# Optimization experiments

Measured on AMD Instinct MI355X. Metric: run time of the kernel, lower is better.

Reference implementation:

```python
import jax, jax.numpy as jnp
import numpy as np

B, N, E, D, L, NC = 64, 128, 1024, 256, 2, 7
BETA = 0.3  # args.diffloss
BIG = 1e30  # mask_logic constant (score - (1-adj)*1e30), as in torch source lineage


def setup_inputs():
    key = jax.random.key(0)
    ks = iter(jax.random.split(key, 48))
    def p(shape, s=0.02):
        return jax.random.normal(next(ks), shape, jnp.float32) * s
    inp = {}
    inp["features"] = jax.random.normal(next(ks), (B, N, E), jnp.float32)
    inp["adj_1"] = jax.random.randint(next(ks), (B, N, N), 0, 2, jnp.int32)
    inp["adj_2"] = jax.random.randint(next(ks), (B, N, N), 0, 2, jnp.int32)
    inp["s_mask"] = jax.random.randint(next(ks), (B, N, N), 0, 2, jnp.int32)
    inp["s_mask_onehot"] = jnp.zeros((B, N, N, 2), jnp.int32)
    inp["lengths"] = jnp.full((B,), N, jnp.int32)
    inp["fc1_w"] = p((D, E)); inp["fc1_b"] = jnp.zeros((D,), jnp.float32)
    # GRUCell params (torch layout: weight_ih (3D,D) order r,z,n)
    for nm in ["gcs", "gps", "gcl", "gpl"]:
        inp[nm + "_wih"] = p((L, 3 * D, D)); inp[nm + "_whh"] = p((L, 3 * D, D))
        inp[nm + "_bih"] = jnp.zeros((L, 3 * D), jnp.float32)
        inp[nm + "_bhh"] = jnp.zeros((L, 3 * D), jnp.float32)
    # GatDot params per layer: linear1 (Q proj), linear2 (K proj)
    for nm in ["gats", "gatl"]:
        inp[nm + "_wq"] = p((L, D, D)); inp[nm + "_bq"] = jnp.zeros((L, D), jnp.float32)
        inp[nm + "_wk"] = p((L, D, D)); inp[nm + "_bk"] = jnp.zeros((L, D), jnp.float32)
    inp["affine1"] = p((2 * D, 2 * D), 0.05)
    inp["affine2"] = p((2 * D, 2 * D), 0.05)
    IN = 4 * D + E  # hidden*2*2 + emb_dim
    inp["mlp_w1"] = p((D, IN)); inp["mlp_b1"] = jnp.zeros((D,), jnp.float32)
    inp["mlp_w2"] = p((D, D)); inp["mlp_b2"] = jnp.zeros((D,), jnp.float32)
    inp["out_w"] = p((NC, D)); inp["out_b"] = jnp.zeros((NC,), jnp.float32)
    return inp


def gru_cell(x, h, wih, whh, bih, bhh):
    gi = x @ wih.T + bih
    gh = h @ whh.T + bhh
    ir, iz, in_ = jnp.split(gi, 3, axis=-1)
    hr, hz, hn = jnp.split(gh, 3, axis=-1)
    r = jax.nn.sigmoid(ir + hr)
    z = jax.nn.sigmoid(iz + hz)
    n = jnp.tanh(in_ + r * hn)
    return (1.0 - z) * n + z * h


def dag_pass(H_in, adj, gat, cpar, ppar):
    """Sequential DAG pass: per-utterance masked dot-product gather + GRU-C/GRU-P."""
    wq, bq, wk, bk = gat
    n = H_in.shape[1]
    idx = jnp.arange(n)

    def step(carry, inp):
        H1, Kb = carry            # H1: [B,N,D] written prefix; Kb = linear2(H1)
        i, x, arow = inp          # x: [B,D], arow: [B,N]
        q = x @ wq.T + bq
        scores = jnp.einsum('bnd,bd->bn', Kb, q)
        # torch: alpha - (1-adj)*1e30 over prefix :i; positions >= i excluded
        logits = scores - (1.0 - arow) * BIG - (idx >= i).astype(scores.dtype) * (2.0 * BIG)
        w = jax.nn.softmax(logits, axis=-1)
        M = jnp.einsum('bn,bnd->bd', w, H1)  # exactly 0 at i==0 (buffer zeros)
        C = gru_cell(x, M, *cpar)   # grus_c(input=x, hidden=M)
        P = gru_cell(M, x, *ppar)   # grus_p(input=M, hidden=x)
        h = C + P
        H1 = jax.lax.dynamic_update_slice(H1, h[:, None, :], (0, i, 0))
        Kb = jax.lax.dynamic_update_slice(Kb, (h @ wk.T + bk)[:, None, :], (0, i, 0))
        return (H1, Kb), None

    init = (jnp.zeros_like(H_in), jnp.zeros_like(H_in))
    xs = (idx, jnp.swapaxes(H_in, 0, 1), jnp.swapaxes(adj, 0, 1))
    (H1, _), _ = jax.lax.scan(step, init, xs)
    return H1


def diff_loss_fn(a, b):
    # orthogonality (DSN-style) loss between short/long channel features
    x = a.reshape(-1, a.shape[-1])
    y = b.reshape(-1, b.shape[-1])
    x = x - x.mean(axis=0, keepdims=True)
    y = y - y.mean(axis=0, keepdims=True)
    x = x / (jnp.linalg.norm(x, axis=1, keepdims=True) + 1e-6)
    y = y / (jnp.linalg.norm(y, axis=1, keepdims=True) + 1e-6)
    return jnp.mean((x.T @ y) ** 2)


def _forward(features, adj_1, adj_2,
             fc1_w, fc1_b,
             gcs_wih, gcs_whh, gcs_bih, gcs_bhh,
             gps_wih, gps_whh, gps_bih, gps_bhh,
             gcl_wih, gcl_whh, gcl_bih, gcl_bhh,
             gpl_wih, gpl_whh, gpl_bih, gpl_bhh,
             gats_wq, gats_bq, gats_wk, gats_bk,
             gatl_wq, gatl_bq, gatl_wk, gatl_bk,
             affine1, affine2,
             mlp_w1, mlp_b1, mlp_w2, mlp_b2, out_w, out_b):
    adj1 = adj_1.astype(jnp.float32)
    adj2 = adj_2.astype(jnp.float32)
    H0 = jax.nn.relu(features @ fc1_w.T + fc1_b)
    H0r = jax.nn.relu(features[:, ::-1] @ fc1_w.T + fc1_b)
    adj1r = adj1[:, ::-1, ::-1]
    adj2r = adj2[:, ::-1, ::-1]

    def channel(adjf, adjb, wq, bq, wk, bk, cwih, cwhh, cbih, cbhh, pwih, pwhh, pbih, pbhh):
        Hf, Hb = H0, H0r
        outs = []
        for l in range(L):
            gat = (wq[l], bq[l], wk[l], bk[l])
            cp = (cwih[l], cwhh[l], cbih[l], cbhh[l])
            pp = (pwih[l], pwhh[l], pbih[l], pbhh[l])
            Hf = dag_pass(Hf, adjf, gat, cp, pp)
            Hb = dag_pass(Hb, adjb, gat, cp, pp)
            outs.append(jnp.concatenate([Hf, Hb], axis=-1))  # no flip-back (as in source)
        return outs

    cs = channel(adj1, adj1r, gats_wq, gats_bq, gats_wk, gats_bk,
                 gcs_wih, gcs_whh, gcs_bih, gcs_bhh, gps_wih, gps_whh, gps_bih, gps_bhh)
    cl = channel(adj2, adj2r, gatl_wq, gatl_bq, gatl_wk, gatl_bk,
                 gcl_wih, gcl_whh, gcl_bih, gcl_bhh, gpl_wih, gpl_whh, gpl_bih, gpl_bhh)

    dloss = sum(diff_loss_fn(a, b) for a, b in zip(cs, cl)) * BETA

    HS, HL = cs[-1], cl[-1]  # [B,N,2D]
    A1 = jax.nn.softmax(jnp.einsum('bnd,de,bme->bnm', HS, affine1, HL), axis=-1)
    A2 = jax.nn.softmax(jnp.einsum('bnd,de,bme->bnm', HL, affine2, HS), axis=-1)
    HSn = jnp.einsum('bnm,bmd->bnd', A1, HL)
    HLn = jnp.einsum('bnm,bmd->bnd', A2, HS)

    Hfin = jnp.concatenate([features, HSn, HLn], axis=-1)  # in_dim = emb + 4D
    h = jax.nn.relu(Hfin @ mlp_w1.T + mlp_b1)
    h = jax.nn.relu(h @ mlp_w2.T + mlp_b2)
    logits = h @ out_w.T + out_b
    return logits, dloss


def reference(features, adj_1, adj_2, s_mask, s_mask_onehot, lengths,
              fc1_w, fc1_b,
              gcs_wih, gcs_whh, gcs_bih, gcs_bhh,
              gps_wih, gps_whh, gps_bih, gps_bhh,
              gcl_wih, gcl_whh, gcl_bih, gcl_bhh,
              gpl_wih, gpl_whh, gpl_bih, gpl_bhh,
              gats_wq, gats_bq, gats_wk, gats_bk,
              gatl_wq, gatl_bq, gatl_wk, gatl_bk,
              affine1, affine2,
              mlp_w1, mlp_b1, mlp_w2, mlp_b2, out_w, out_b):
    # s_mask / s_mask_onehot / lengths unused for attn_type='dotprod', no_rel_attn=True, nodal_att_type=None
    return _forward(features, adj_1, adj_2,
                    fc1_w, fc1_b,
                    gcs_wih, gcs_whh, gcs_bih, gcs_bhh,
                    gps_wih, gps_whh, gps_bih, gps_bhh,
                    gcl_wih, gcl_whh, gcl_bih, gcl_bhh,
                    gpl_wih, gpl_whh, gpl_bih, gpl_bhh,
                    gats_wq, gats_bq, gats_wk, gats_bk,
                    gatl_wq, gatl_bq, gatl_wk, gatl_bk,
                    affine1, affine2,
                    mlp_w1, mlp_b1, mlp_w2, mlp_b2, out_w, out_b)
```

## Files before the change

### kernel.cpp

```cpp
#include <hip/hip_runtime.h>
#include <hip/hip_fp16.h>
#include <math.h>

#define SB   64
#define SN   128
#define SE   1024
#define SD   256
#define SD2  512
#define SD3  768
#define SIN  2048
#define SNC  7
#define SBN  8192
#define CS   16

#define L_HS   0
#define L_GK   65536
#define L_XH   114688
#define L_QH   122880
#define L_ADJ  131072
#define L_MH   139264
#define L_LGP  139776
#define L_WGT  140800
#define L_S0   141312
#define SMEM_BYTES 141376

typedef _Float16 h2v __attribute__((ext_vector_type(2)));

__device__ __forceinline__ float wsum(float v){
#pragma unroll
  for (int o = 32; o; o >>= 1) v += __shfl_xor(v, o);
  return v;
}
__device__ __forceinline__ float sigm(float x){ return 1.f/(1.f + expf(-x)); }

__device__ __forceinline__ unsigned short f2h(float f){
  return __half_as_ushort(__float2half_rn(f));
}
__device__ __forceinline__ float h2f_(unsigned short u){
  return __half2float(__ushort_as_half(u));
}
__device__ __forceinline__ h2v u2h(unsigned u){
  union { unsigned u; h2v h; } c; c.u = u; return c.h;
}
__device__ __forceinline__ float dot8d(uint4 w, uint4 m, float acc){
  acc = __builtin_amdgcn_fdot2(u2h(w.x), u2h(m.x), acc, false);
  acc = __builtin_amdgcn_fdot2(u2h(w.y), u2h(m.y), acc, false);
  acc = __builtin_amdgcn_fdot2(u2h(w.z), u2h(m.z), acc, false);
  acc = __builtin_amdgcn_fdot2(u2h(w.w), u2h(m.w), acc, false);
  return acc;
}

template<bool BKMAJ, bool BIAS, bool RELU, bool ACC>
__global__ __launch_bounds__(256)
void gemm_k(const float* __restrict__ A, const float* __restrict__ Bm,
            const float* __restrict__ bias, float* __restrict__ C,
            int Nn, int K, int lda, int ldb, int ldc,
            long sA, long sB, long sC)
{
  __shared__ float As[16][132];
  __shared__ float Bs[16][68];
  const int t  = threadIdx.x;
  const int tx = t & 15, ty = t >> 4;
  const float* Ab = A + (long)blockIdx.z * sA;
  const float* Bb = Bm + (long)blockIdx.z * sB;
  float* Cb = C + (long)blockIdx.z * sC;
  const int m0 = blockIdx.y * 128, n0 = blockIdx.x * 64;
  float acc[8][4];
#pragma unroll
  for (int i = 0; i < 8; ++i)
#pragma unroll
    for (int j = 0; j < 4; ++j) acc[i][j] = 0.f;

  const int am = t >> 1, ak = (t & 1) * 8;
  int bn_ = 0, bk_ = 0;
  if (BKMAJ) { bk_ = t >> 4; bn_ = (t & 15) * 4; }
  else       { bn_ = t >> 2; bk_ = (t & 3) * 4; }

  for (int k0 = 0; k0 < K; k0 += 16) {
    const float4 a0 = *(const float4*)(Ab + (long)(m0 + am) * lda + k0 + ak);
    const float4 a1 = *(const float4*)(Ab + (long)(m0 + am) * lda + k0 + ak + 4);
    float4 b0;
    if (BKMAJ) b0 = *(const float4*)(Bb + (long)(k0 + bk_) * ldb + n0 + bn_);
    else       b0 = *(const float4*)(Bb + (long)(n0 + bn_) * ldb + k0 + bk_);
    __syncthreads();
    As[ak+0][am] = a0.x; As[ak+1][am] = a0.y; As[ak+2][am] = a0.z; As[ak+3][am] = a0.w;
    As[ak+4][am] = a1.x; As[ak+5][am] = a1.y; As[ak+6][am] = a1.z; As[ak+7][am] = a1.w;
    if (BKMAJ) { *(float4*)&Bs[bk_][bn_] = b0; }
    else { Bs[bk_+0][bn_] = b0.x; Bs[bk_+1][bn_] = b0.y; Bs[bk_+2][bn_] = b0.z; Bs[bk_+3][bn_] = b0.w; }
    __syncthreads();
#pragma unroll
    for (int kk = 0; kk < 16; ++kk) {
      float av[8], bv[4];
      *(float4*)&av[0] = *(const float4*)&As[kk][ty*8];
      *(float4*)&av[4] = *(const float4*)&As[kk][ty*8+4];
      *(float4*)&bv[0] = *(const float4*)&Bs[kk][tx*4];
#pragma unroll
      for (int ii = 0; ii < 8; ++ii)
#pragma unroll
        for (int jj = 0; jj < 4; ++jj)
          acc[ii][jj] = fmaf(av[ii], bv[jj], acc[ii][jj]);
    }
  }
#pragma unroll
  for (int ii = 0; ii < 8; ++ii) {
#pragma unroll
    for (int jj = 0; jj < 4; ++jj) {
      float v = acc[ii][jj];
      if (BIAS) v += bias[n0 + tx*4 + jj];
      const long ci = (long)(m0 + ty*8 + ii) * ldc + n0 + tx*4 + jj;
      if (ACC) v += Cb[ci];
      if (RELU) v = fmaxf(v, 0.f);
      Cb[ci] = v;
    }
  }
}

__global__ void spread_k(const float* __restrict__ src, float* __restrict__ xf,
                         float* __restrict__ xr)
{
  const int r = blockIdx.x, t = threadIdx.x;
  const int b = r >> 7, n = r & 127;
  const float v = src[(long)r * SD + t];
  xf[((long)(n * 64 + b)) * SD + t] = v;
  xr[((long)((127 - n) * 64 + b)) * SD + t] = v;
}

struct PTArgs { const float* wc[4]; const float* wp[4]; unsigned short* Wt; };
__global__ void packT_k(PTArgs a)
{
  const int kb8 = blockIdx.x, cd = blockIdx.y, t = threadIdx.x;
#pragma unroll
  for (int p = 0; p < 6; ++p) {
    const int r = t + 256 * p;
    const float* src = (r < 768) ? (a.wc[cd] + (long)r * SD)
                                 : (a.wp[cd] + (long)(r - 768) * SD);
    const float4 v0 = *(const float4*)(src + kb8 * 8);
    const float4 v1 = *(const float4*)(src + kb8 * 8 + 4);
    uint4 o;
    o.x = (unsigned)f2h(v0.x) | ((unsigned)f2h(v0.y) << 16);
    o.y = (unsigned)f2h(v0.z) | ((unsigned)f2h(v0.w) << 16);
    o.z = (unsigned)f2h(v1.x) | ((unsigned)f2h(v1.y) << 16);
    o.w = (unsigned)f2h(v1.z) | ((unsigned)f2h(v1.w) << 16);
    *(uint4*)(a.Wt + (((size_t)cd * 32 + kb8) * 1536 + r) * 8) = o;
  }
}

__global__ void s0_k(const float* __restrict__ Q, const float* __restrict__ bk,
                     float* __restrict__ S0)
{
  const int r = blockIdx.x * 4 + (threadIdx.x >> 6), lane = threadIdx.x & 63;
  const float4 q  = *(const float4*)(Q + (long)r * SD + lane * 4);
  const float4 kb = *(const float4*)(bk + lane * 4);
  float p = q.x*kb.x + q.y*kb.y + q.z*kb.z + q.w*kb.w;
  p = wsum(p);
  if (lane == 0) S0[r] = p;
}

struct StepArgs {
  const float* Qt[4]; const float* S0[4];
  const int* adj[4]; int rev[4];
  const float* bc[4];  const float* bp[4];
  const float* bgc[4]; const float* bgp[4];
  const float* X[4];
  float* H1[4];
  unsigned short* Hh;
  const unsigned short* Wt;
  const unsigned short* Wgk;
  int ldX, s0;
};
__global__ __launch_bounds__(256, 1) void step_chunk_k(StepArgs a)
{
  extern __shared__ __align__(16) char dsm[];
  unsigned short* Hs  = (unsigned short*)(dsm + L_HS);
  unsigned short* GKh = (unsigned short*)(dsm + L_GK);
  unsigned short* Xh  = (unsigned short*)(dsm + L_XH);
  unsigned short* Qh  = (unsigned short*)(dsm + L_QH);
  float* adjc = (float*)(dsm + L_ADJ);
  unsigned short* Mh  = (unsigned short*)(dsm + L_MH);
  float* lgp  = (float*)(dsm + L_LGP);
  float* wgt  = (float*)(dsm + L_WGT);
  float* s0s  = (float*)(dsm + L_S0);

  const int blk = blockIdx.x;
  const int cd = blk & 3, b = blk >> 2;
  const int t = threadIdx.x, j = t;
  const int ldX = a.ldX, c0 = a.s0;
  const float* Xp  = a.X[cd];
  float* H1 = a.H1[cd];
  unsigned short* Hg = a.Hh + ((size_t)(cd * 64 + b)) * 128 * 256;
  const float* Qtp = a.Qt[cd];
  const float* S0p = a.S0[cd];
  const int*   adjp = a.adj[cd];
  const int    rev  = a.rev[cd];

  const float bc0 = a.bc[cd][j],  bc1 = a.bc[cd][256+j],  bc2 = a.bc[cd][512+j];
  const float bp0 = a.bp[cd][j],  bp1 = a.bp[cd][256+j],  bp2 = a.bp[cd][512+j];

#pragma unroll
  for (int s = 0; s < CS; ++s) {
    Xh[s*256 + t] = f2h(Xp[((long)(c0+s)*64 + b)*ldX + t]);
    Qh[s*256 + t] = f2h(Qtp[((long)(c0+s)*64 + b)*SD + t]);
  }
  for (int z = t; z < CS*128; z += 256) {
    const int s = z >> 7, n = z & 127;
    const int i = c0 + s;
    int av = 0;
    if (i > 0) {
      const int ii = rev ? (SN-1-i) : i;
      const int nn = rev ? (SN-1-n) : n;
      av = adjp[((long)b*SN + ii)*SN + nn];
    }
    adjc[z] = (float)av;
  }
  if (t < CS) s0s[t] = S0p[(c0+t)*64 + b];
  for (int o = t*16; o < c0*512; o += 4096) {
    const uint4 v = *(const uint4*)((const char*)Hg + o);
    const int row = o >> 9, d2 = o & 511;
    *(uint4*)((char*)Hs + row*512 + (d2 ^ ((row & 31) << 4))) = v;
  }
  __syncthreads();

  {
    float gacc[6][CS];
#pragma unroll
    for (int g = 0; g < 6; ++g)
#pragma unroll
      for (int s = 0; s < CS; ++s) gacc[g][s] = 0.f;
    const unsigned short* wbase = a.Wgk + ((size_t)cd*32*1536 + j)*8;
    for (int kb8 = 0; kb8 < 32; ++kb8) {
      const uint4* wr = (const uint4*)(wbase + (size_t)kb8*12288);
      uint4 w[6];
#pragma unroll
      for (int g = 0; g < 6; ++g) w[g] = wr[g*256];
#pragma unroll
      for (int s = 0; s < CS; ++s) {
        const uint4 x8 = *(const uint4*)&Xh[s*256 + kb8*8];
#pragma unroll
        for (int g = 0; g < 6; ++g)
          gacc[g][s] = dot8d(w[g], x8, gacc[g][s]);
      }
    }
#pragma unroll
    for (int g = 0; g < 6; ++g) {
      const float bg = (g < 3) ? a.bgc[cd][g*256 + j] : a.bgp[cd][(g-3)*256 + j];
#pragma unroll
      for (int s = 0; s < CS; ++s)
        GKh[s*1536 + g*256 + j] = f2h(gacc[g][s] + bg);
    }
  }
  __syncthreads();

  for (int s = 0; s < CS; ++s) {
    const int i = c0 + s;
    float mreg = 0.f;
    if (i == 0) {
      Mh[t] = 0;
      __syncthreads();
    } else {
      {
        const int n = t & 127, hi = t >> 7;
        if (n < i) {
          const char* hrow = (const char*)Hs + n*512;
          const int cx = (n & 31) << 4;
          const unsigned short* qrow = Qh + s*256 + hi*128;
          float acc = 0.f;
#pragma unroll
          for (int k = 0; k < 16; ++k) {
            const uint4 hv = *(const uint4*)(hrow + (((hi*16 + k)*16) ^ cx));
            const uint4 qv = *(const uint4*)(qrow + k*8);
            acc = dot8d(hv, qv, acc);
          }
          lgp[t] = acc;
        }
      }
      __syncthreads();
      if (t < 64) {
        const float s0v = s0s[s];
        const int l = t;
        const float lg0 = lgp[l]      + lgp[128 + l];
        const float lg1 = lgp[64 + l] + lgp[192 + l];
        const float v0 = (l < i)    ? (lg0 + s0v - (1.f - adjc[s*128+l]   )*1e30f) : -3.0e38f;
        const float v1 = (l+64 < i) ? (lg1 + s0v - (1.f - adjc[s*128+l+64])*1e30f) : -3.0e38f;
        float mx = fmaxf(v0, v1);
#pragma unroll
        for (int o = 32; o; o >>= 1) mx = fmaxf(mx, __shfl_xor(mx, o));
        const float e0 = (l < i)    ? expf(v0 - mx) : 0.f;
        const float e1 = (l+64 < i) ? expf(v1 - mx) : 0.f;
        float sum = e0 + e1;
#pragma unroll
        for (int o = 32; o; o >>= 1) sum += __shfl_xor(sum, o);
        const float inv = 1.f / sum;
        if (l < i)    wgt[l]    = e0 * inv;
        if (l+64 < i) wgt[l+64] = e1 * inv;
      }
      __syncthreads();
      {
        float m0 = 0.f, m1 = 0.f, m2 = 0.f, m3 = 0.f;
        int n = 0;
        for (; n + 4 <= i; n += 4) {
          m0 = fmaf(wgt[n+0], h2f_(Hs[(n+0)*256 + (j ^ (((n+0)&31)<<3))]), m0);
          m1 = fmaf(wgt[n+1], h2f_(Hs[(n+1)*256 + (j ^ (((n+1)&31)<<3))]), m1);
          m2 = fmaf(wgt[n+2], h2f_(Hs[(n+2)*256 + (j ^ (((n+2)&31)<<3))]), m2);
          m3 = fmaf(wgt[n+3], h2f_(Hs[(n+3)*256 + (j ^ (((n+3)&31)<<3))]), m3);
        }
        for (; n < i; ++n)
          m0 = fmaf(wgt[n], h2f_(Hs[n*256 + (j ^ ((n&31)<<3))]), m0);
        mreg = (m0 + m1) + (m2 + m3);
        Mh[t] = f2h(mreg);
      }
      __syncthreads();
    }

    float g0 = 0.f, g1 = 0.f, g2 = 0.f, g3 = 0.f, g4 = 0.f, g5 = 0.f;
    {
      const unsigned short* wb = a.Wt + ((size_t)cd*32*1536 + j)*8;
      const uint4* wr0 = (const uint4*)wb;
      uint4 c0r = wr0[0], c1r = wr0[256], c2r = wr0[512],
            c3r = wr0[768], c4r = wr0[1024], c5r = wr0[1280];
#pragma unroll 4
      for (int kb8 = 0; kb8 < 32; ++kb8) {
        uint4 n0 = c0r, n1 = c1r, n2 = c2r, n3 = c3r, n4 = c4r, n5 = c5r;
        if (kb8 < 31) {
          const uint4* wn = (const uint4*)(wb + (size_t)(kb8+1)*12288);
          n0 = wn[0]; n1 = wn[256]; n2 = wn[512];
          n3 = wn[768]; n4 = wn[1024]; n5 = wn[1280];
        }
        const uint4 m8 = *(const uint4*)&Mh[kb8*8];
        g0 = dot8d(c0r, m8, g0);
        g1 = dot8d(c1r, m8, g1);
        g2 = dot8d(c2r, m8, g2);
        g3 = dot8d(c3r, m8, g3);
        g4 = dot8d(c4r, m8, g4);
        g5 = dot8d(c5r, m8, g5);
        c0r = n0; c1r = n1; c2r = n2; c3r = n3; c4r = n4; c5r = n5;
      }
    }
    {
      const int sb = s*1536;
      const float gic_r = h2f_(GKh[sb + j]);
      const float gic_z = h2f_(GKh[sb + 256 + j]);
      const float gic_n = h2f_(GKh[sb + 512 + j]);
      const float ghp_r = h2f_(GKh[sb + 768 + j]);
      const float ghp_z = h2f_(GKh[sb + 1024 + j]);
      const float ghp_n = h2f_(GKh[sb + 1280 + j]);
      const float xj = Xp[((long)i*64 + b)*ldX + j];
      const float rC = sigm(gic_r + g0 + bc0);
      const float zC = sigm(gic_z + g1 + bc1);
      const float nC = tanhf(gic_n + rC * (g2 + bc2));
      const float Cc = (1.f - zC) * nC + zC * mreg;
      const float rP = sigm(g3 + bp0 + ghp_r);
      const float zP = sigm(g4 + bp1 + ghp_z);
      const float nP = tanhf(g5 + bp2 + rP * ghp_n);
      const float hval = Cc + (1.f - zP) * nP + zP * xj;
      H1[((long)i*64 + b)*SD2 + j] = hval;
      const unsigned short hh = f2h(hval);
      Hs[i*256 + (j ^ ((i & 31) << 3))] = hh;
      Hg[(size_t)i*256 + j] = hh;
    }
    __syncthreads();
  }
}

__global__ void zero_k(float* p, long n)
{
  for (long idx = (long)blockIdx.x * 256 + threadIdx.x; idx < n; idx += (long)gridDim.x * 256)
    p[idx] = 0.f;
}

__global__ void colmean_k(const float* __restrict__ X, float* __restrict__ mean)
{
  __shared__ float red[256];
  const int c = blockIdx.x * 64 + (threadIdx.x & 63), rq = threadIdx.x >> 6;
  const int r0 = blockIdx.y * 256;
  float acc = 0.f;
  for (int r = r0 + rq; r < r0 + 256; r += 4) acc += X[(long)r * SD2 + c];
  red[threadIdx.x] = acc;
  __syncthreads();
  if (threadIdx.x < 64) {
    const float s = red[threadIdx.x] + red[64 + threadIdx.x] + red[128 + threadIdx.x] + red[192 + threadIdx.x];
    atomicAdd(&mean[c], s * (1.f / 8192.f));
  }
}

__global__ void rownorm_k(const float* __restrict__ X, const float* __restrict__ mean,
                          float* __restrict__ inv)
{
  const int r = blockIdx.x * 4 + (threadIdx.x >> 6), lane = threadIdx.x & 63;
  const float* xp = X + (long)r * SD2 + lane * 8;
  const float4 v0 = *(const float4*)xp;
  const float4 v1 = *(const float4*)(xp + 4);
  const float4 m0 = *(const float4*)(mean + lane * 8);
  const float4 m1 = *(const float4*)(mean + lane * 8 + 4);
  float ss = 0.f, d;
  d = v0.x - m0.x; ss += d*d;  d = v0.y - m0.y; ss += d*d;
  d = v0.z - m0.z; ss += d*d;  d = v0.w - m0.w; ss += d*d;
  d = v1.x - m1.x; ss += d*d;  d = v1.y - m1.y; ss += d*d;
  d = v1.z - m1.z; ss += d*d;  d = v1.w - m1.w; ss += d*d;
  ss = wsum(ss);
  if (lane == 0) inv[r] = 1.f / (sqrtf(ss) + 1e-6f);
}

__global__ __launch_bounds__(256)
void gpart_k(const float* __restrict__ X, const float* __restrict__ Y,
             const float* __restrict__ mx, const float* __restrict__ my,
             const float* __restrict__ ix, const float* __restrict__ iy,
             float* __restrict__ G)
{
  __shared__ float As[16][68];
  __shared__ float Bs[16][68];
  __shared__ float mxs[64], mys[64];
  const int t = threadIdx.x, tx = t & 15, ty = t >> 4;
  const int ci = blockIdx.y * 64, cj = blockIdx.x * 64;
  if (t < 64) { mxs[t] = mx[ci + t]; mys[t] = my[cj + t]; }
  float acc[4][4];
#pragma unroll
  for (int ii = 0; ii < 4; ++ii)
#pragma unroll
    for (int jj = 0; jj < 4; ++jj) acc[ii][jj] = 0.f;
  const int rl = t >> 4, c4 = (t & 15) * 4;
  __syncthreads();
  const int kend = blockIdx.z * 512 + 512;
  for (int kb = blockIdx.z * 512; kb < kend; kb += 16) {
    const int r = kb + rl;
    const float4 xv = *(const float4*)(X + (long)r * SD2 + ci + c4);
    const float4 yv = *(const float4*)(Y + (long)r * SD2 + cj + c4);
    const float vx = ix[r], vy = iy[r];
    __syncthreads();
    As[rl][c4+0] = (xv.x - mxs[c4+0]) * vx; As[rl][c4+1] = (xv.y - mxs[c4+1]) * vx;
    As[rl][c4+2] = (xv.z - mxs[c4+2]) * vx; As[rl][c4+3] = (xv.w - mxs[c4+3]) * vx;
    Bs[rl][c4+0] = (yv.x - mys[c4+0]) * vy; Bs[rl][c4+1] = (yv.y - mys[c4+1]) * vy;
    Bs[rl][c4+2] = (yv.z - mys[c4+2]) * vy; Bs[rl][c4+3] = (yv.w - mys[c4+3]) * vy;
    __syncthreads();
#pragma unroll
    for (int kk = 0; kk < 16; ++kk) {
      float av[4], bv[4];
      *(float4*)&av[0] = *(const float4*)&As[kk][ty*4];
      *(float4*)&bv[0] = *(const float4*)&Bs[kk][tx*4];
#pragma unroll
      for (int ii = 0; ii < 4; ++ii)
#pragma unroll
        for (int jj = 0; jj < 4; ++jj)
          acc[ii][jj] = fmaf(av[ii], bv[jj], acc[ii][jj]);
    }
  }
#pragma unroll
  for (int ii = 0; ii < 4; ++ii)
#pragma unroll
    for (int jj = 0; jj < 4; ++jj)
      atomicAdd(&G[(long)(ci + ty*4 + ii) * SD2 + cj + tx*4 + jj], acc[ii][jj]);
}

__global__ void sqsum_k(const float* __restrict__ G, float* __restrict__ dl)
{
  __shared__ float red[4];
  float s = 0.f;
  const long base = (long)blockIdx.x * 1024;
#pragma unroll
  for (int it = 0; it < 4; ++it) { const float v = G[base + it*256 + threadIdx.x]; s += v*v; }
  s = wsum(s);
  const int lane = threadIdx.x & 63, wv = threadIdx.x >> 6;
  if (lane == 0) red[wv] = s;
  __syncthreads();
  if (threadIdx.x == 0) atomicAdd(dl, red[0] + red[1] + red[2] + red[3]);
}

__global__ void smax_k(float* __restrict__ S)
{
  const int r = blockIdx.x * 4 + (threadIdx.x >> 6), lane = threadIdx.x & 63;
  float* p = S + (long)r * SN;
  const float v0 = p[lane], v1 = p[lane + 64];
  float mx = fmaxf(v0, v1);
#pragma unroll
  for (int o = 32; o; o >>= 1) mx = fmaxf(mx, __shfl_xor(mx, o));
  const float e0 = expf(v0 - mx), e1 = expf(v1 - mx);
  float s = e0 + e1;
#pragma unroll
  for (int o = 32; o; o >>= 1) s += __shfl_xor(s, o);
  const float inv = 1.f / s;
  p[lane] = e0 * inv; p[lane + 64] = e1 * inv;
}

__global__ void head_k(const float* __restrict__ H, const float* __restrict__ W,
                       const float* __restrict__ bo, float* __restrict__ out)
{
  const int r = blockIdx.x * 4 + (threadIdx.x >> 6), lane = threadIdx.x & 63;
  const float4 h = *(const float4*)(H + (long)r * SD + lane * 4);
#pragma unroll
  for (int c = 0; c < SNC; ++c) {
    const float4 w = *(const float4*)(W + (long)c * SD + lane * 4);
    float p = h.x*w.x + h.y*w.y + h.z*w.z + h.w*w.w;
    p = wsum(p);
    if (lane == 0) out[(long)r * SNC + c] = p + bo[c];
  }
}

__global__ void fin_k(const float* __restrict__ dl, float* __restrict__ out)
{
  out[0] = (dl[0] + dl[1]) * (0.3f / (512.f * 512.f));
}

extern "C" void kernel_launch(void* const* d_in, const int* in_sizes, int n_in,
                              void* d_out, int out_size, void* d_ws, size_t ws_size,
                              hipStream_t stream)
{
  (void)in_sizes; (void)n_in; (void)out_size; (void)ws_size;

  static bool attr_set = false;
  if (!attr_set) {
    hipFuncSetAttribute(reinterpret_cast<const void*>(step_chunk_k),
                        hipFuncAttributeMaxDynamicSharedMemorySize, SMEM_BYTES);
    attr_set = true;
  }

  const float* F    = (const float*)d_in[0];
  const int*   adj1 = (const int*)  d_in[1];
  const int*   adj2 = (const int*)  d_in[2];
  const float* fc1w = (const float*)d_in[6];
  const float* fc1b = (const float*)d_in[7];
  const float *g_wih[4], *g_whh[4], *g_bih[4], *g_bhh[4];
  for (int g = 0; g < 4; ++g) {
    g_wih[g] = (const float*)d_in[8 + g*4 + 0];
    g_whh[g] = (const float*)d_in[8 + g*4 + 1];
    g_bih[g] = (const float*)d_in[8 + g*4 + 2];
    g_bhh[g] = (const float*)d_in[8 + g*4 + 3];
  }
  const float* gat_wq[2] = {(const float*)d_in[24], (const float*)d_in[28]};
  const float* gat_bq[2] = {(const float*)d_in[25], (const float*)d_in[29]};
  const float* gat_wk[2] = {(const float*)d_in[26], (const float*)d_in[30]};
  const float* gat_bk[2] = {(const float*)d_in[27], (const float*)d_in[31]};
  const float* aff1 = (const float*)d_in[32];
  const float* aff2 = (const float*)d_in[33];
  const float* mw1  = (const float*)d_in[34];
  const float* mb1  = (const float*)d_in[35];
  const float* mw2  = (const float*)d_in[36];
  const float* mb2  = (const float*)d_in[37];
  const float* ow   = (const float*)d_in[38];
  const float* ob   = (const float*)d_in[39];
  float* out = (float*)d_out;

  float* ws = (float*)d_ws;
  size_t off = 0;
  auto take = [&](size_t nf){ float* p = ws + off; off += nf; return p; };
  float* region = take(22552576);
  float* X0f  = region;
  float* X0r  = region + 2097152;
  float* Qtb  = region + 4194304;
  float* Qtmp = region + 12582912;
  float* Htmp = region + 14680064;
  float* T  = region;
  float* Sb = region + 4194304;
  float* HH = region + 5242880;
  float* h1 = region + 9437184;
  float* h2 = region + 11534336;
  float* Ocat[2][2];
  for (int c = 0; c < 2; ++c) for (int l = 0; l < 2; ++l) Ocat[c][l] = take(4194304);
  float* S0b   = take(32768);
  unsigned short* WtB  = (unsigned short*)take(786432);
  unsigned short* WgkB = (unsigned short*)take(786432);
  unsigned short* HhB  = (unsigned short*)take(4194304);
  float* meanx = take(512);
  float* meany = take(512);
  float* invx  = take(8192);
  float* invy  = take(8192);
  float* dl    = take(8);
  float* Gbuf  = take(262144);

  gemm_k<false,true,true,false><<<dim3(4,64,1),256,0,stream>>>(
      F, fc1w, fc1b, Htmp, SD, SE, SE, SE, SD, 0,0,0);
  spread_k<<<SBN,256,0,stream>>>(Htmp, X0f, X0r);

  for (int l = 0; l < 2; ++l) {
    PTArgs pt, pg; StepArgs sta;
    sta.ldX = l ? SD2 : SD;
    sta.Wt = WtB; sta.Wgk = WgkB; sta.Hh = HhB;
    const int ldX = sta.ldX;
    for (int cd = 0; cd < 4; ++cd) {
      const int ch = cd >> 1;
      const float* X = (l == 0) ? ((cd & 1) ? X0r : X0f)
                                : (Ocat[ch][0] + (cd & 1) * SD);
      const float* wq   = gat_wq[ch] + l * SD * SD;
      const float* bq   = gat_bq[ch] + l * SD;
      const float* wk   = gat_wk[ch] + l * SD * SD;
      const float* bk   = gat_bk[ch] + l * SD;
      const float* cwih = g_wih[ch*2+0] + l * SD3 * SD;
      const float* cwhh = g_whh[ch*2+0] + l * SD3 * SD;
      const float* cbih = g_bih[ch*2+0] + l * SD3;
      const float* cbhh = g_bhh[ch*2+0] + l * SD3;
      const float* pwih = g_wih[ch*2+1] + l * SD3 * SD;
      const float* pwhh = g_whh[ch*2+1] + l * SD3 * SD;
      const float* pbih = g_bih[ch*2+1] + l * SD3;
      const float* pbhh = g_bhh[ch*2+1] + l * SD3;
      pt.wc[cd] = cwhh; pt.wp[cd] = pwih;
      pg.wc[cd] = cwih; pg.wp[cd] = pwhh;
      gemm_k<false,true,false,false><<<dim3(4,64,1),256,0,stream>>>(
          X, wq, bq, Qtmp, SD, SD, ldX, SD, SD, 0,0,0);
      gemm_k<true,false,false,false><<<dim3(4,64,1),256,0,stream>>>(
          Qtmp, wk, nullptr, Qtb + (size_t)cd*2097152, SD, SD, SD, SD, SD, 0,0,0);
      s0_k<<<SBN/4,256,0,stream>>>(Qtmp, bk, S0b + cd*SBN);
      float* H1mut = Ocat[ch][l] + (cd & 1) * SD;
      sta.Qt[cd] = Qtb + (size_t)cd*2097152;
      sta.S0[cd] = S0b + cd*SBN;
      sta.H1[cd] = H1mut;
      sta.adj[cd] = ch ? adj2 : adj1; sta.rev[cd] = cd & 1;
      sta.bc[cd]  = cbhh; sta.bp[cd]  = pbih;
      sta.bgc[cd] = cbih; sta.bgp[cd] = pbhh;
      sta.X[cd] = X;
    }
    pt.Wt = WtB;  packT_k<<<dim3(32,4),256,0,stream>>>(pt);
    pg.Wt = WgkB; packT_k<<<dim3(32,4),256,0,stream>>>(pg);

    for (int s0 = 0; s0 < SN; s0 += CS) {
      sta.s0 = s0;
      step_chunk_k<<<256,256,SMEM_BYTES,stream>>>(sta);
    }
  }

  zero_k<<<1,256,0,stream>>>(dl, 2);
  for (int l = 0; l < 2; ++l) {
    zero_k<<<4,256,0,stream>>>(meanx, 1024);
    colmean_k<<<dim3(8,32,1),256,0,stream>>>(Ocat[0][l], meanx);
    colmean_k<<<dim3(8,32,1),256,0,stream>>>(Ocat[1][l], meany);
    rownorm_k<<<SBN/4,256,0,stream>>>(Ocat[0][l], meanx, invx);
    rownorm_k<<<SBN/4,256,0,stream>>>(Ocat[1][l], meany, invy);
    zero_k<<<256,256,0,stream>>>(Gbuf, (long)SD2*SD2);
    gpart_k<<<dim3(8,8,16),256,0,stream>>>(Ocat[0][l], Ocat[1][l], meanx, meany, invx, invy, Gbuf);
    sqsum_k<<<256,256,0,stream>>>(Gbuf, dl + l);
  }

  gemm_k<true,false,false,false><<<dim3(8,64,1),256,0,stream>>>(
      Ocat[0][1], aff1, nullptr, T, SD2, SD2, SD2, SD2, SD2, 0,0,0);
  gemm_k<false,false,false,false><<<dim3(2,1,64),256,0,stream>>>(
      T, Ocat[1][1], nullptr, Sb, SN, SD2, 64*SD2, 64*SD2, SN, SD2, SD2, (long)SN*SN);
  smax_k<<<SBN/4,256,0,stream>>>(Sb);
  gemm_k<true,false,false,false><<<dim3(8,1,64),256,0,stream>>>(
      Sb, Ocat[1][1], nullptr, HH, SD2, SN, SN, 64*SD2, SD2, (long)SN*SN, SD2, (long)SN*SD2);
  gemm_k<false,true,false,false><<<dim3(4,64,1),256,0,stream>>>(
      F, mw1, mb1, h1, SD, SE, SE, SIN, SD, 0,0,0);
  gemm_k<false,false,false,true><<<dim3(4,64,1),256,0,stream>>>(
      HH, mw1 + 1024, nullptr, h1, SD, SD2, SD2, SIN, SD, 0,0,0);
  gemm_k<true,false,false,false><<<dim3(8,64,1),256,0,stream>>>(
      Ocat[1][1], aff2, nullptr, T, SD2, SD2, SD2, SD2, SD2, 0,0,0);
  gemm_k<false,false,false,false><<<dim3(2,1,64),256,0,stream>>>(
      T, Ocat[0][1], nullptr, Sb, SN, SD2, 64*SD2, 64*SD2, SN, SD2, SD2, (long)SN*SN);
  smax_k<<<SBN/4,256,0,stream>>>(Sb);
  gemm_k<true,false,false,false><<<dim3(8,1,64),256,0,stream>>>(
      Sb, Ocat[0][1], nullptr, HH, SD2, SN, SN, 64*SD2, SD2, (long)SN*SN, SD2, (long)SN*SD2);
  gemm_k<false,false,true,true><<<dim3(4,64,1),256,0,stream>>>(
      HH, mw1 + 1536, nullptr, h1, SD, SD2, SD2, SIN, SD, 0,0,0);
  gemm_k<false,true,true,false><<<dim3(4,64,1),256,0,stream>>>(
      h1, mw2, mb2, h2, SD, SD, SD, SD, SD, 0,0,0);
  head_k<<<SBN/4,256,0,stream>>>(h2, ow, ob, out);
  fin_k<<<1,1,0,stream>>>(dl, out + SBN * SNC);
}
```

Baseline: 4.743 ms.

## Double step kernel block size, splitting GRU-C and GRU-P gates across thread halves

```diff
diff --git a/kernel.cpp b/kernel.cpp
--- a/kernel.cpp
+++ b/kernel.cpp
@@ -20,9 +20,11 @@
 #define L_ADJ  131072
 #define L_MH   139264
 #define L_LGP  139776
-#define L_WGT  140800
-#define L_S0   141312
-#define SMEM_BYTES 141376
+#define L_MP   141824
+#define L_WGT  143872
+#define L_PBUF 144384
+#define L_S0   145408
+#define SMEM_BYTES 145472
 
 typedef _Float16 h2v __attribute__((ext_vector_type(2)));
 
@@ -168,7 +170,7 @@
   const unsigned short* Wgk;
   int ldX, s0;
 };
-__global__ __launch_bounds__(256, 1) void step_chunk_k(StepArgs a)
+__global__ __launch_bounds__(512, 1) void step_chunk_k(StepArgs a)
 {
   extern __shared__ __align__(16) char dsm[];
   unsigned short* Hs  = (unsigned short*)(dsm + L_HS);
@@ -178,12 +180,15 @@
   float* adjc = (float*)(dsm + L_ADJ);
   unsigned short* Mh  = (unsigned short*)(dsm + L_MH);
   float* lgp  = (float*)(dsm + L_LGP);
+  float* Mp   = (float*)(dsm + L_MP);
   float* wgt  = (float*)(dsm + L_WGT);
+  float* pbuf = (float*)(dsm + L_PBUF);
   float* s0s  = (float*)(dsm + L_S0);
 
   const int blk = blockIdx.x;
   const int cd = blk & 3, b = blk >> 2;
-  const int t = threadIdx.x, j = t;
+  const int t = threadIdx.x;
+  const int half = t >> 8, j = t & 255;
   const int ldX = a.ldX, c0 = a.s0;
   const float* Xp  = a.X[cd];
   float* H1 = a.H1[cd];
@@ -193,15 +198,23 @@
   const int*   adjp = a.adj[cd];
   const int    rev  = a.rev[cd];
 
-  const float bc0 = a.bc[cd][j],  bc1 = a.bc[cd][256+j],  bc2 = a.bc[cd][512+j];
-  const float bp0 = a.bp[cd][j],  bp1 = a.bp[cd][256+j],  bp2 = a.bp[cd][512+j];
-
-#pragma unroll
-  for (int s = 0; s < CS; ++s) {
-    Xh[s*256 + t] = f2h(Xp[((long)(c0+s)*64 + b)*ldX + t]);
-    Qh[s*256 + t] = f2h(Qtp[((long)(c0+s)*64 + b)*SD + t]);
-  }
-  for (int z = t; z < CS*128; z += 256) {
+  float eb0, eb1, eb2, gb0, gb1, gb2;
+  if (half == 0) {
+    eb0 = a.bc[cd][j];  eb1 = a.bc[cd][256+j];  eb2 = a.bc[cd][512+j];
+    gb0 = a.bgc[cd][j]; gb1 = a.bgc[cd][256+j]; gb2 = a.bgc[cd][512+j];
+  } else {
+    eb0 = a.bp[cd][j];  eb1 = a.bp[cd][256+j];  eb2 = a.bp[cd][512+j];
+    gb0 = a.bgp[cd][j]; gb1 = a.bgp[cd][256+j]; gb2 = a.bgp[cd][512+j];
+  }
+  const unsigned short* wb   = a.Wt  + ((size_t)cd*32*1536 + half*768 + j)*8;
+  const unsigned short* wbgk = a.Wgk + ((size_t)cd*32*1536 + half*768 + j)*8;
+
+  for (int z = t; z < CS*256; z += 512) {
+    const int s = z >> 8, c = z & 255;
+    Xh[z] = f2h(Xp[((long)(c0+s)*64 + b)*ldX + c]);
+    Qh[z] = f2h(Qtp[((long)(c0+s)*64 + b)*SD + c]);
+  }
+  for (int z = t; z < CS*128; z += 512) {
     const int s = z >> 7, n = z & 127;
     const int i = c0 + s;
     int av = 0;
@@ -213,7 +226,7 @@
     adjc[z] = (float)av;
   }
   if (t < CS) s0s[t] = S0p[(c0+t)*64 + b];
-  for (int o = t*16; o < c0*512; o += 4096) {
+  for (int o = t*16; o < c0*512; o += 8192) {
     const uint4 v = *(const uint4*)((const char*)Hg + o);
     const int row = o >> 9, d2 = o & 511;
     *(uint4*)((char*)Hs + row*512 + (d2 ^ ((row & 31) << 4))) = v;
@@ -221,52 +234,49 @@
   __syncthreads();
 
   {
-    float gacc[6][CS];
-#pragma unroll
-    for (int g = 0; g < 6; ++g)
+    float gacc[3][CS];
+#pragma unroll
+    for (int g = 0; g < 3; ++g)
 #pragma unroll
       for (int s = 0; s < CS; ++s) gacc[g][s] = 0.f;
-    const unsigned short* wbase = a.Wgk + ((size_t)cd*32*1536 + j)*8;
     for (int kb8 = 0; kb8 < 32; ++kb8) {
-      const uint4* wr = (const uint4*)(wbase + (size_t)kb8*12288);
-      uint4 w[6];
-#pragma unroll
-      for (int g = 0; g < 6; ++g) w[g] = wr[g*256];
+      const uint4* wr = (const uint4*)(wbgk + (size_t)kb8*12288);
+      const uint4 w0 = wr[0], w1 = wr[256], w2 = wr[512];
 #pragma unroll
       for (int s = 0; s < CS; ++s) {
         const uint4 x8 = *(const uint4*)&Xh[s*256 + kb8*8];
-#pragma unroll
-        for (int g = 0; g < 6; ++g)
-          gacc[g][s] = dot8d(w[g], x8, gacc[g][s]);
-      }
-    }
-#pragma unroll
-    for (int g = 0; g < 6; ++g) {
-      const float bg = (g < 3) ? a.bgc[cd][g*256 + j] : a.bgp[cd][(g-3)*256 + j];
+        gacc[0][s] = dot8d(w0, x8, gacc[0][s]);
+        gacc[1][s] = dot8d(w1, x8, gacc[1][s]);
+        gacc[2][s] = dot8d(w2, x8, gacc[2][s]);
+      }
+    }
+    const float gb[3] = {gb0, gb1, gb2};
+#pragma unroll
+    for (int g = 0; g < 3; ++g)
 #pragma unroll
       for (int s = 0; s < CS; ++s)
-        GKh[s*1536 + g*256 + j] = f2h(gacc[g][s] + bg);
-    }
+        GKh[s*1536 + (half*3 + g)*256 + j] = f2h(gacc[g][s] + gb[g]);
   }
   __syncthreads();
 
   for (int s = 0; s < CS; ++s) {
     const int i = c0 + s;
+    const float xj = Xp[((long)i*64 + b)*ldX + j];
     float mreg = 0.f;
     if (i == 0) {
-      Mh[t] = 0;
+      if (t < 256) Mh[t] = 0;
       __syncthreads();
     } else {
       {
-        const int n = t & 127, hi = t >> 7;
+        const int n = t & 127, q4 = t >> 7;
         if (n < i) {
           const char* hrow = (const char*)Hs + n*512;
           const int cx = (n & 31) << 4;
-          const unsigned short* qrow = Qh + s*256 + hi*128;
+          const unsigned short* qrow = Qh + s*256 + q4*64;
           float acc = 0.f;
 #pragma unroll
-          for (int k = 0; k < 16; ++k) {
-            const uint4 hv = *(const uint4*)(hrow + (((hi*16 + k)*16) ^ cx));
+          for (int k = 0; k < 8; ++k) {
+            const uint4 hv = *(const uint4*)(hrow + (((q4*8 + k)*16) ^ cx));
             const uint4 qv = *(const uint4*)(qrow + k*8);
             acc = dot8d(hv, qv, acc);
           }
@@ -277,8 +287,8 @@
       if (t < 64) {
         const float s0v = s0s[s];
         const int l = t;
-        const float lg0 = lgp[l]      + lgp[128 + l];
-        const float lg1 = lgp[64 + l] + lgp[192 + l];
+        const float lg0 = (lgp[l]      + lgp[128 + l]) + (lgp[256 + l] + lgp[384 + l]);
+        const float lg1 = (lgp[64 + l] + lgp[192 + l]) + (lgp[320 + l] + lgp[448 + l]);
         const float v0 = (l < i)    ? (lg0 + s0v - (1.f - adjc[s*128+l]   )*1e30f) : -3.0e38f;
         const float v1 = (l+64 < i) ? (lg1 + s0v - (1.f - adjc[s*128+l+64])*1e30f) : -3.0e38f;
         float mx = fmaxf(v0, v1);
@@ -296,68 +306,71 @@
       __syncthreads();
       {
         float m0 = 0.f, m1 = 0.f, m2 = 0.f, m3 = 0.f;
-        int n = 0;
-        for (; n + 4 <= i; n += 4) {
-          m0 = fmaf(wgt[n+0], h2f_(Hs[(n+0)*256 + (j ^ (((n+0)&31)<<3))]), m0);
-          m1 = fmaf(wgt[n+1], h2f_(Hs[(n+1)*256 + (j ^ (((n+1)&31)<<3))]), m1);
-          m2 = fmaf(wgt[n+2], h2f_(Hs[(n+2)*256 + (j ^ (((n+2)&31)<<3))]), m2);
-          m3 = fmaf(wgt[n+3], h2f_(Hs[(n+3)*256 + (j ^ (((n+3)&31)<<3))]), m3);
+        int n = half;
+        for (; n + 6 < i; n += 8) {
+          m0 = fmaf(wgt[n],   h2f_(Hs[(n  )*256 + (j ^ (((n  )&31)<<3))]), m0);
+          m1 = fmaf(wgt[n+2], h2f_(Hs[(n+2)*256 + (j ^ (((n+2)&31)<<3))]), m1);
+          m2 = fmaf(wgt[n+4], h2f_(Hs[(n+4)*256 + (j ^ (((n+4)&31)<<3))]), m2);
+          m3 = fmaf(wgt[n+6], h2f_(Hs[(n+6)*256 + (j ^ (((n+6)&31)<<3))]), m3);
         }
-        for (; n < i; ++n)
+        for (; n < i; n += 2)
           m0 = fmaf(wgt[n], h2f_(Hs[n*256 + (j ^ ((n&31)<<3))]), m0);
-        mreg = (m0 + m1) + (m2 + m3);
-        Mh[t] = f2h(mreg);
+        Mp[t] = (m0 + m1) + (m2 + m3);
       }
       __syncthreads();
-    }
-
-    float g0 = 0.f, g1 = 0.f, g2 = 0.f, g3 = 0.f, g4 = 0.f, g5 = 0.f;
+      if (half == 0) {
+        mreg = Mp[j] + Mp[256 + j];
+        Mh[j] = f2h(mreg);
+      }
+      __syncthreads();
+    }
+
+    float g0 = 0.f, g1 = 0.f, g2 = 0.f;
     {
-      const unsigned short* wb = a.Wt + ((size_t)cd*32*1536 + j)*8;
       const uint4* wr0 = (const uint4*)wb;
-      uint4 c0r = wr0[0], c1r = wr0[256], c2r = wr0[512],
-            c3r = wr0[768], c4r = wr0[1024], c5r = wr0[1280];
+      uint4 c0r = wr0[0], c1r = wr0[256], c2r = wr0[512];
 #pragma unroll 4
       for (int kb8 = 0; kb8 < 32; ++kb8) {
-        uint4 n0 = c0r, n1 = c1r, n2 = c2r, n3 = c3r, n4 = c4r, n5 = c5r;
+        uint4 n0 = c0r, n1 = c1r, n2 = c2r;
         if (kb8 < 31) {
           const uint4* wn = (const uint4*)(wb + (size_t)(kb8+1)*12288);
           n0 = wn[0]; n1 = wn[256]; n2 = wn[512];
-          n3 = wn[768]; n4 = wn[1024]; n5 = wn[1280];
         }
         const uint4 m8 = *(const uint4*)&Mh[kb8*8];
         g0 = dot8d(c0r, m8, g0);
         g1 = dot8d(c1r, m8, g1);
         g2 = dot8d(c2r, m8, g2);
-        g3 = dot8d(c3r, m8, g3);
-        g4 = dot8d(c4r, m8, g4);
-        g5 = dot8d(c5r, m8, g5);
-        c0r = n0; c1r = n1; c2r = n2; c3r = n3; c4r = n4; c5r = n5;
-      }
-    }
+        c0r = n0; c1r = n1; c2r = n2;
+      }
+    }
+
     {
       const int sb = s*1536;
-      const float gic_r = h2f_(GKh[sb + j]);
-      const float gic_z = h2f_(GKh[sb + 256 + j]);
-      const float gic_n = h2f_(GKh[sb + 512 + j]);
-      const float ghp_r = h2f_(GKh[sb + 768 + j]);
-      const float ghp_z = h2f_(GKh[sb + 1024 + j]);
-      const float ghp_n = h2f_(GKh[sb + 1280 + j]);
-      const float xj = Xp[((long)i*64 + b)*ldX + j];
-      const float rC = sigm(gic_r + g0 + bc0);
-      const float zC = sigm(gic_z + g1 + bc1);
-      const float nC = tanhf(gic_n + rC * (g2 + bc2));
-      const float Cc = (1.f - zC) * nC + zC * mreg;
-      const float rP = sigm(g3 + bp0 + ghp_r);
-      const float zP = sigm(g4 + bp1 + ghp_z);
-      const float nP = tanhf(g5 + bp2 + rP * ghp_n);
-      const float hval = Cc + (1.f - zP) * nP + zP * xj;
-      H1[((long)i*64 + b)*SD2 + j] = hval;
-      const unsigned short hh = f2h(hval);
-      Hs[i*256 + (j ^ ((i & 31) << 3))] = hh;
-      Hg[(size_t)i*256 + j] = hh;
-    }
-    __syncthreads();
+      if (half == 1) {
+        const float ghp_r = h2f_(GKh[sb + 768 + j]);
+        const float ghp_z = h2f_(GKh[sb + 1024 + j]);
+        const float ghp_n = h2f_(GKh[sb + 1280 + j]);
+        const float rP = sigm(g0 + eb0 + ghp_r);
+        const float zP = sigm(g1 + eb1 + ghp_z);
+        const float nP = tanhf(g2 + eb2 + rP * ghp_n);
+        pbuf[j] = (1.f - zP) * nP + zP * xj;
+      }
+      __syncthreads();
+      if (half == 0) {
+        const float gic_r = h2f_(GKh[sb + j]);
+        const float gic_z = h2f_(GKh[sb + 256 + j]);
+        const float gic_n = h2f_(GKh[sb + 512 + j]);
+        const float rC = sigm(gic_r + g0 + eb0);
+        const float zC = sigm(gic_z + g1 + eb1);
+        const float nC = tanhf(gic_n + rC * (g2 + eb2));
+        const float hval = (1.f - zC) * nC + zC * mreg + pbuf[j];
+        H1[((long)i*64 + b)*SD2 + j] = hval;
+        const unsigned short hh = f2h(hval);
+        Hs[i*256 + (j ^ ((i & 31) << 3))] = hh;
+        Hg[(size_t)i*256 + j] = hh;
+      }
+      __syncthreads();
+    }
   }
 }
 
@@ -611,7 +624,7 @@
 
     for (int s0 = 0; s0 < SN; s0 += CS) {
       sta.s0 = s0;
-      step_chunk_k<<<256,256,SMEM_BYTES,stream>>>(sta);
+      step_chunk_k<<<256,512,SMEM_BYTES,stream>>>(sta);
     }
   }
 
```

Result: faster. 4.553 ms (-4.0%).
